# Performance work log

Hardware: AMD Instinct MI355X
Metric: run time of the kernel (lower is better)

The kernel has to match this reference:

```python
import jax, jax.numpy as jnp
import numpy as np

B, L, D = 16, 1024, 256  # batch, c_len == q_len (required by the expand/add in the source), 2*d_model


def mask_logits(x, m):
    # Faithful to the source's (unusual) masking: x*m + x*(1-m)*1e30
    return x * m + x * (1.0 - m) * 1e30


def setup_inputs() -> dict:
    key = jax.random.key(0)
    k = jax.random.split(key, 7)
    c = jax.random.normal(k[0], (B, L, D), dtype=jnp.float32)
    q = jax.random.normal(k[1], (B, L, D), dtype=jnp.float32)
    c_mask = jnp.ones((B, 1, L), dtype=jnp.float32)
    q_mask = jnp.ones((B, 1, L), dtype=jnp.float32)
    # Learned parameters (nn.Parameter zeros in the source; random here so the test is non-degenerate)
    c_weight = jax.random.normal(k[2], (D, 1), dtype=jnp.float32) * 0.05
    q_weight = jax.random.normal(k[3], (D, 1), dtype=jnp.float32) * 0.05
    cq_weight = jax.random.normal(k[4], (1, 1, D), dtype=jnp.float32) * 0.05
    bias = jnp.zeros((1,), dtype=jnp.float32)
    return {"c": c, "q": q, "c_mask": c_mask, "q_mask": q_mask,
            "c_weight": c_weight, "q_weight": q_weight,
            "cq_weight": cq_weight, "bias": bias}


def reference(c, q, c_mask, q_mask, c_weight, q_weight, cq_weight, bias):
    # Dropout treated as identity (inference) for a deterministic reference.
    s0 = jnp.matmul(c, c_weight)                      # [B, L, 1] -> broadcasts over q_len
    s1 = jnp.swapaxes(jnp.matmul(c, q_weight), 1, 2)  # [B, 1, L] (source uses c here, not q)
    s2 = jnp.einsum('bid,bjd->bij', c * cq_weight, q) # [B, L, L]
    S = s0 + s1 + s2 + bias                           # trilinear similarity
    S1 = jax.nn.softmax(mask_logits(S, q_mask), axis=-1)              # [B, Lc, Lq]
    C2Q = jnp.matmul(S1, q)                                           # [B, Lc, D]
    # torch F.softmax with no dim on a 3D tensor defaults to dim=0 (legacy behavior) -> axis=0
    S2 = jax.nn.softmax(mask_logits(jnp.swapaxes(S, 1, 2), c_mask), axis=0)  # [B, Lq, Lc]
    S2 = jnp.matmul(S1, S2)                                           # [B, Lc, Lc]
    Q2C = jnp.matmul(S2, c)                                           # [B, Lc, D]
    # torch.cat default dim=0 -> [4B, Lc, D]
    return jnp.concatenate((c, C2Q, c * C2Q, c * Q2C), axis=0)
```

## Files before the change

kernel.cpp:

```cpp
#include <hip/hip_runtime.h>

typedef __bf16 bf16;
typedef _Float16 f16;
typedef __attribute__((ext_vector_type(8))) __bf16 bf16x8;
typedef __attribute__((ext_vector_type(4))) __bf16 bf16x4;
typedef __attribute__((ext_vector_type(8))) _Float16 f16x8;
typedef __attribute__((ext_vector_type(4))) _Float16 f16x4;
typedef __attribute__((ext_vector_type(4))) float f32x4;

constexpr int Bn = 16, Ln = 1024, Dn = 256;

__device__ __forceinline__ float maskf(float m) { return m + (1.0f - m) * 1e30f; }

__device__ __forceinline__ void gload16(const void* g, void* l) {
  __builtin_amdgcn_global_load_lds((const __attribute__((address_space(1))) void*)g,
                                   (__attribute__((address_space(3))) void*)l, 16, 0, 0);
}

__device__ __forceinline__ void stageB128(const bf16* __restrict__ B, int ldb, int k0,
                                          bf16* lB, int tid, int wid) {
#pragma unroll
  for (int p = 0; p < 2; ++p) {
    int c0 = tid + (p << 8);
    int row = c0 >> 2, kk = (c0 & 3) << 3;
    gload16(B + (size_t)row * ldb + k0 + kk, lB + ((p << 8) + (wid << 6)) * 8);
  }
}

__device__ __forceinline__ void stageSwz64(const bf16* __restrict__ G, int ldg, int k0,
                                           bf16* L, int tid, int wid) {
#pragma unroll
  for (int p = 0; p < 2; ++p) {
    int u = tid + (p << 8);
    int row = u >> 3, s = u & 7;
    int kk = ((s ^ (row & 7)) << 3);
    gload16(G + (size_t)row * ldg + k0 + kk, L + ((p << 8) + (wid << 6)) * 8);
  }
}
__device__ __forceinline__ void stageSwz128(const bf16* __restrict__ G, int ldg, int k0,
                                            bf16* L, int tid, int wid) {
#pragma unroll
  for (int p = 0; p < 4; ++p) {
    int u = tid + (p << 8);
    int row = u >> 3, s = u & 7;
    int kk = ((s ^ (row & 7)) << 3);
    gload16(G + (size_t)row * ldg + k0 + kk, L + ((p << 8) + (wid << 6)) * 8);
  }
}

__device__ __forceinline__ const bf16* swzp(const bf16* L, int row, int slot) {
  return L + row * 64 + ((slot ^ (row & 7)) << 3);
}

__global__ __launch_bounds__(256) void k_prep2(
    const float* __restrict__ c, const float* __restrict__ q,
    const float* __restrict__ cw, const float* __restrict__ qw,
    const float* __restrict__ cqw, bf16* __restrict__ cm, bf16* __restrict__ qb,
    bf16* __restrict__ cT, bf16* __restrict__ qT,
    float* __restrict__ s0, float* __restrict__ s1, float* __restrict__ outc) {
  __shared__ __align__(16) bf16 tc[32][264];
  __shared__ __align__(16) bf16 tq[32][264];
  int blk = blockIdx.x;
  int b = blk >> 5;
  int l0 = (blk & 31) << 5;
  int t = threadIdx.x;
  int rl = t >> 3;
  int c0 = (t & 7) << 5;
  int grow = b * Ln + l0 + rl;
  size_t base = (size_t)grow * Dn + c0;
  float4 cv[8], qv[8];
#pragma unroll
  for (int k = 0; k < 8; ++k) {
    cv[k] = *(const float4*)&c[base + k * 4];
    qv[k] = *(const float4*)&q[base + k * 4];
  }
  float d0 = 0.f, d1 = 0.f;
#pragma unroll
  for (int k = 0; k < 8; ++k) {
    float4 w = *(const float4*)&cw[c0 + k * 4];
    float4 u = *(const float4*)&qw[c0 + k * 4];
    d0 += cv[k].x * w.x + cv[k].y * w.y + cv[k].z * w.z + cv[k].w * w.w;
    d1 += cv[k].x * u.x + cv[k].y * u.y + cv[k].z * u.z + cv[k].w * u.w;
  }
  d0 += __shfl_xor(d0, 1); d0 += __shfl_xor(d0, 2); d0 += __shfl_xor(d0, 4);
  d1 += __shfl_xor(d1, 1); d1 += __shfl_xor(d1, 2); d1 += __shfl_xor(d1, 4);
  if ((t & 7) == 0) { s0[grow] = d0; s1[grow] = d1; }
#pragma unroll
  for (int k = 0; k < 8; ++k) *(float4*)&outc[base + k * 4] = cv[k];
#pragma unroll
  for (int k2 = 0; k2 < 4; ++k2) {
    float4 m0 = *(const float4*)&cqw[c0 + k2 * 8];
    float4 m1 = *(const float4*)&cqw[c0 + k2 * 8 + 4];
    bf16x8 vm, vq, vc;
#pragma unroll
    for (int e = 0; e < 8; ++e) {
      float cvv = ((const float*)&cv[k2 * 2 + (e >> 2)])[e & 3];
      float qvv = ((const float*)&qv[k2 * 2 + (e >> 2)])[e & 3];
      float mw = (e < 4) ? ((const float*)&m0)[e] : ((const float*)&m1)[e - 4];
      vm[e] = (bf16)(cvv * mw);
      vq[e] = (bf16)qvv;
      vc[e] = (bf16)cvv;
    }
    *(bf16x8*)&cm[base + k2 * 8] = vm;
    *(bf16x8*)&qb[base + k2 * 8] = vq;
    *(bf16x8*)&tc[rl][c0 + k2 * 8] = vc;
    *(bf16x8*)&tq[rl][c0 + k2 * 8] = vq;
  }
  __syncthreads();
  int d = t;
  size_t tb = ((size_t)b * Dn + d) * Ln + l0;
  bf16x8 o[4];
#pragma unroll
  for (int j = 0; j < 4; ++j)
#pragma unroll
    for (int e = 0; e < 8; ++e) o[j][e] = tc[j * 8 + e][d];
#pragma unroll
  for (int j = 0; j < 4; ++j) *(bf16x8*)&cT[tb + j * 8] = o[j];
#pragma unroll
  for (int j = 0; j < 4; ++j)
#pragma unroll
    for (int e = 0; e < 8; ++e) o[j][e] = tq[j * 8 + e][d];
#pragma unroll
  for (int j = 0; j < 4; ++j) *(bf16x8*)&qT[tb + j * 8] = o[j];
}

__global__ __launch_bounds__(256) void g_s(const bf16* __restrict__ Am,
                                           const bf16* __restrict__ Bm,
                                           const float* __restrict__ s0,
                                           const float* __restrict__ s1,
                                           const float* __restrict__ bias,
                                           f16* __restrict__ S) {
  __shared__ __align__(16) bf16 lds[2][256 * 32];
  int f = blockIdx.x;
  int o = (f & 7) * 128 + (f >> 3);
  int bx = o & 7, by = (o >> 3) & 7, b = o >> 6;
  const bf16* Ab = Am + (size_t)b * Ln * Dn + (size_t)by * 128 * Dn;
  const bf16* Bb = Bm + (size_t)b * Ln * Dn + (size_t)bx * 128 * Dn;
  const int tid = threadIdx.x, wid = tid >> 6, lane = tid & 63;
  const int r = lane & 15, h = lane >> 4, wr = wid >> 1, wc = wid & 1;
  f32x4 acc[4][4];
  f32x4 zero = {0.f, 0.f, 0.f, 0.f};
#pragma unroll
  for (int i = 0; i < 4; ++i)
#pragma unroll
    for (int j = 0; j < 4; ++j) acc[i][j] = zero;

  stageB128(Ab, Dn, 0, &lds[0][0], tid, wid);
  stageB128(Bb, Dn, 0, &lds[0][128 * 32], tid, wid);
  __syncthreads();
  for (int t = 0; t < 8; ++t) {
    int cur = t & 1;
    if (t < 7) {
      stageB128(Ab, Dn, (t + 1) * 32, &lds[cur ^ 1][0], tid, wid);
      stageB128(Bb, Dn, (t + 1) * 32, &lds[cur ^ 1][128 * 32], tid, wid);
    }
    const bf16* lA = &lds[cur][0];
    const bf16* lB = &lds[cur][128 * 32];
    bf16x8 av[4], bv[4];
#pragma unroll
    for (int i = 0; i < 4; ++i) {
      av[i] = *(const bf16x8*)(lA + ((wr << 6) + (i << 4) + r) * 32 + (h << 3));
      bv[i] = *(const bf16x8*)(lB + ((wc << 6) + (i << 4) + r) * 32 + (h << 3));
    }
#pragma unroll
    for (int i = 0; i < 4; ++i)
#pragma unroll
      for (int j = 0; j < 4; ++j)
        acc[i][j] = __builtin_amdgcn_mfma_f32_16x16x32_bf16(av[i], bv[j], acc[i][j], 0, 0, 0);
    __syncthreads();
  }
  int grow = by * 128 + wr * 64, gcol = bx * 128 + wc * 64;
  float bvv = bias[0];
  size_t sb = (size_t)b * Ln * Ln;
#pragma unroll
  for (int j = 0; j < 4; ++j) {
    int n = gcol + j * 16 + r;
    float v1 = s1[b * Ln + n];
#pragma unroll
    for (int i = 0; i < 4; ++i) {
      int mb = grow + i * 16 + h * 4;
#pragma unroll
      for (int g = 0; g < 4; ++g) {
        float v0 = s0[b * Ln + mb + g];
        S[sb + (size_t)(mb + g) * Ln + n] = (f16)(acc[i][j][g] + v0 + v1 + bvv);
      }
    }
  }
}

__global__ __launch_bounds__(256) void k_rowsoftmax(const f16* __restrict__ S,
                                                    const float* __restrict__ qmask,
                                                    bf16* __restrict__ P1) {
  int t = threadIdx.x;
  int row = blockIdx.x * 4 + (t >> 6);
  int b = row >> 10;
  int lane = t & 63;
  const f16* Sr = S + (size_t)row * Ln;
  const float* qm = qmask + (size_t)b * Ln;
  float v[16];
  float mx = -3.4e38f;
#pragma unroll
  for (int p = 0; p < 2; ++p) {
    f16x8 x = ((const f16x8*)Sr)[lane + (p << 6)];
    float4 m0 = ((const float4*)qm)[(lane + (p << 6)) * 2];
    float4 m1 = ((const float4*)qm)[(lane + (p << 6)) * 2 + 1];
    float mm[8] = {m0.x, m0.y, m0.z, m0.w, m1.x, m1.y, m1.z, m1.w};
#pragma unroll
    for (int e = 0; e < 8; ++e) {
      float xv = (float)x[e] * maskf(mm[e]);
      v[8 * p + e] = xv;
      mx = fmaxf(mx, xv);
    }
  }
#pragma unroll
  for (int off = 32; off; off >>= 1) mx = fmaxf(mx, __shfl_xor(mx, off));
  float sum = 0.f;
#pragma unroll
  for (int k = 0; k < 16; ++k) {
    v[k] = __expf(v[k] - mx);
    sum += v[k];
  }
#pragma unroll
  for (int off = 32; off; off >>= 1) sum += __shfl_xor(sum, off);
  float inv = 1.0f / sum;
  bf16* Pr = P1 + (size_t)row * Ln;
#pragma unroll
  for (int p = 0; p < 2; ++p) {
    bf16x8 o;
#pragma unroll
    for (int e = 0; e < 8; ++e) o[e] = (bf16)(v[8 * p + e] * inv);
    ((bf16x8*)Pr)[lane + (p << 6)] = o;
  }
}

__global__ __launch_bounds__(256) void k_bp2(const f16* __restrict__ S,
                                             const float* __restrict__ cmask,
                                             bf16* __restrict__ P2) {
  __shared__ __align__(16) bf16 tile[16][32][36];
  int i0 = blockIdx.y * 32, j0 = blockIdx.x * 32;
  int t = threadIdx.x;
  int ti = t >> 3, tj4 = (t & 7) << 2;
  int i = i0 + ti;
  const f16* Sp = S + (size_t)i * Ln + j0 + tj4;
  float fm[16];
#pragma unroll
  for (int b = 0; b < 16; ++b) fm[b] = maskf(cmask[b * Ln + i]);
  float m[4] = {-3.4e38f, -3.4e38f, -3.4e38f, -3.4e38f};
#pragma unroll
  for (int b = 0; b < 16; ++b) {
    f16x4 u = *(const f16x4*)(Sp + (size_t)b * Ln * Ln);
#pragma unroll
    for (int g = 0; g < 4; ++g) m[g] = fmaxf(m[g], (float)u[g] * fm[b]);
  }
  float s[4] = {0.f, 0.f, 0.f, 0.f};
#pragma unroll
  for (int b = 0; b < 16; ++b) {
    f16x4 u = *(const f16x4*)(Sp + (size_t)b * Ln * Ln);
#pragma unroll
    for (int g = 0; g < 4; ++g) s[g] += __expf((float)u[g] * fm[b] - m[g]);
  }
#pragma unroll
  for (int g = 0; g < 4; ++g) s[g] = 1.0f / s[g];
#pragma unroll
  for (int b = 0; b < 16; ++b) {
    f16x4 u = *(const f16x4*)(Sp + (size_t)b * Ln * Ln);
#pragma unroll
    for (int g = 0; g < 4; ++g)
      tile[b][tj4 + g][ti] = (bf16)(__expf((float)u[g] * fm[b] - m[g]) * s[g]);
  }
  __syncthreads();
  int jl = t >> 3, i4 = (t & 7) << 2;
#pragma unroll
  for (int b = 0; b < 16; ++b) {
    *(bf16x4*)&P2[((size_t)b * Ln + j0 + jl) * Ln + i0 + i4] =
        *(const bf16x4*)&tile[b][jl][i4];
  }
}

__global__ __launch_bounds__(256) void g_t(const bf16* __restrict__ cT,
                                           const bf16* __restrict__ P2,
                                           bf16* __restrict__ TT) {
  __shared__ __align__(16) bf16 lds[2][192 * 64];
  int f = blockIdx.x;
  int o = (f & 7) * 64 + (f >> 3);
  int b = o >> 5, md = (o >> 3) & 3, nb = o & 7;
  const bf16* Ab = cT + (size_t)b * Dn * Ln + (size_t)md * 64 * Ln;
  const bf16* Bb = P2 + (size_t)b * Ln * Ln + (size_t)nb * 128 * Ln;
  const int tid = threadIdx.x, wid = tid >> 6, lane = tid & 63;
  const int r = lane & 15, h = lane >> 4, wr = wid >> 1, wc = wid & 1;
  f32x4 acc[2][4];
  f32x4 zero = {0.f, 0.f, 0.f, 0.f};
#pragma unroll
  for (int i = 0; i < 2; ++i)
#pragma unroll
    for (int j = 0; j < 4; ++j) acc[i][j] = zero;

  stageSwz64(Ab, Ln, 0, &lds[0][0], tid, wid);
  stageSwz128(Bb, Ln, 0, &lds[0][64 * 64], tid, wid);
  __syncthreads();
  for (int t = 0; t < 16; ++t) {
    int cur = t & 1;
    if (t < 15) {
      stageSwz64(Ab, Ln, (t + 1) * 64, &lds[cur ^ 1][0], tid, wid);
      stageSwz128(Bb, Ln, (t + 1) * 64, &lds[cur ^ 1][64 * 64], tid, wid);
    }
    const bf16* lA = &lds[cur][0];
    const bf16* lB = &lds[cur][64 * 64];
#pragma unroll
    for (int kk2 = 0; kk2 < 2; ++kk2) {
      int slot = (kk2 << 2) | h;
      bf16x8 av[2], bv[4];
#pragma unroll
      for (int i = 0; i < 2; ++i)
        av[i] = *(const bf16x8*)swzp(lA, (wr << 5) + (i << 4) + r, slot);
#pragma unroll
      for (int j = 0; j < 4; ++j)
        bv[j] = *(const bf16x8*)swzp(lB, (wc << 6) + (j << 4) + r, slot);
#pragma unroll
      for (int i = 0; i < 2; ++i)
#pragma unroll
        for (int j = 0; j < 4; ++j)
          acc[i][j] = __builtin_amdgcn_mfma_f32_16x16x32_bf16(av[i], bv[j], acc[i][j], 0, 0, 0);
    }
    __syncthreads();
  }
  size_t ob = (size_t)b * Dn * Ln;
  int dbase = md * 64 + wr * 32, cbase = nb * 128 + wc * 64;
#pragma unroll
  for (int i = 0; i < 2; ++i)
#pragma unroll
    for (int j = 0; j < 4; ++j) {
      int n = cbase + j * 16 + r;
#pragma unroll
      for (int g = 0; g < 4; ++g)
        TT[ob + (size_t)(dbase + i * 16 + h * 4 + g) * Ln + n] = (bf16)acc[i][j][g];
    }
}

__global__ __launch_bounds__(256) void g_cq(const bf16* __restrict__ P1,
                                            const bf16* __restrict__ qT,
                                            const bf16* __restrict__ TT,
                                            const float* __restrict__ c,
                                            float* __restrict__ out) {
  __shared__ __align__(16) bf16 lds[2][192 * 64];
  int f = blockIdx.x;
  int o = (f & 7) * 128 + (f >> 3);
  int b = o >> 6, by = (o >> 2) & 15, bx = o & 3;
  const bf16* Ab = P1 + (size_t)b * Ln * Ln + (size_t)by * 64 * Ln;
  const bf16* B1 = qT + (size_t)b * Dn * Ln + (size_t)bx * 64 * Ln;
  const bf16* B2 = TT + (size_t)b * Dn * Ln + (size_t)bx * 64 * Ln;
  const int tid = threadIdx.x, wid = tid >> 6, lane = tid & 63;
  const int r = lane & 15, h = lane >> 4, wr = wid >> 1, wc = wid & 1;
  f32x4 acc1[2][2], acc2[2][2];
  f32x4 zero = {0.f, 0.f, 0.f, 0.f};
#pragma unroll
  for (int i = 0; i < 2; ++i)
#pragma unroll
    for (int j = 0; j < 2; ++j) { acc1[i][j] = zero; acc2[i][j] = zero; }

  stageSwz64(Ab, Ln, 0, &lds[0][0], tid, wid);
  stageSwz64(B1, Ln, 0, &lds[0][4096], tid, wid);
  stageSwz64(B2, Ln, 0, &lds[0][8192], tid, wid);
  __syncthreads();
  for (int t = 0; t < 16; ++t) {
    int cur = t & 1;
    if (t < 15) {
      stageSwz64(Ab, Ln, (t + 1) * 64, &lds[cur ^ 1][0], tid, wid);
      stageSwz64(B1, Ln, (t + 1) * 64, &lds[cur ^ 1][4096], tid, wid);
      stageSwz64(B2, Ln, (t + 1) * 64, &lds[cur ^ 1][8192], tid, wid);
    }
    const bf16* lA = &lds[cur][0];
    const bf16* lB1 = &lds[cur][4096];
    const bf16* lB2 = &lds[cur][8192];
#pragma unroll
    for (int kk2 = 0; kk2 < 2; ++kk2) {
      int slot = (kk2 << 2) | h;
      bf16x8 av[2], bv[2];
#pragma unroll
      for (int i = 0; i < 2; ++i)
        av[i] = *(const bf16x8*)swzp(lA, (wr << 5) + (i << 4) + r, slot);
#pragma unroll
      for (int j = 0; j < 2; ++j)
        bv[j] = *(const bf16x8*)swzp(lB1, (wc << 5) + (j << 4) + r, slot);
#pragma unroll
      for (int i = 0; i < 2; ++i)
#pragma unroll
        for (int j = 0; j < 2; ++j)
          acc1[i][j] = __builtin_amdgcn_mfma_f32_16x16x32_bf16(av[i], bv[j], acc1[i][j], 0, 0, 0);
#pragma unroll
      for (int j = 0; j < 2; ++j)
        bv[j] = *(const bf16x8*)swzp(lB2, (wc << 5) + (j << 4) + r, slot);
#pragma unroll
      for (int i = 0; i < 2; ++i)
#pragma unroll
        for (int j = 0; j < 2; ++j)
          acc2[i][j] = __builtin_amdgcn_mfma_f32_16x16x32_bf16(av[i], bv[j], acc2[i][j], 0, 0, 0);
    }
    __syncthreads();
  }

  int grow = by * 64 + wr * 32, gcol = bx * 64 + wc * 32;
  const float* cb = c + (size_t)b * Ln * Dn;
  float* o1 = out + (size_t)(1 * Bn + b) * Ln * Dn;
  float* o2 = out + (size_t)(2 * Bn + b) * Ln * Dn;
  float* o3 = out + (size_t)(3 * Bn + b) * Ln * Dn;
#pragma unroll
  for (int j = 0; j < 2; ++j) {
    int n = gcol + j * 16 + r;
#pragma unroll
    for (int i = 0; i < 2; ++i) {
      int mb = grow + i * 16 + h * 4;
#pragma unroll
      for (int g = 0; g < 4; ++g) {
        float v1 = acc1[i][j][g];
        float v2 = acc2[i][j][g];
        size_t off = (size_t)(mb + g) * Dn + n;
        float cc = cb[off];
        o1[off] = v1;
        o2[off] = cc * v1;
        o3[off] = cc * v2;
      }
    }
  }
}

extern "C" void kernel_launch(void* const* d_in, const int* in_sizes, int n_in,
                              void* d_out, int out_size, void* d_ws, size_t ws_size,
                              hipStream_t stream) {
  const float* c = (const float*)d_in[0];
  const float* q = (const float*)d_in[1];
  const float* cmask = (const float*)d_in[2];
  const float* qmask = (const float*)d_in[3];
  const float* cw = (const float*)d_in[4];
  const float* qw = (const float*)d_in[5];
  const float* cqw = (const float*)d_in[6];
  const float* bias = (const float*)d_in[7];
  float* out = (float*)d_out;

  char* w = (char*)d_ws;
  f16* S = (f16*)w;       w += (size_t)Bn * Ln * Ln * 2;
  bf16* P1 = (bf16*)w;    w += (size_t)Bn * Ln * Ln * 2;
  bf16* P2 = (bf16*)w;    w += (size_t)Bn * Ln * Ln * 2;
  bf16* cm = (bf16*)w;    w += (size_t)Bn * Ln * Dn * 2;
  bf16* qb = (bf16*)w;    w += (size_t)Bn * Ln * Dn * 2;
  bf16* cT = (bf16*)w;    w += (size_t)Bn * Dn * Ln * 2;
  bf16* qT = (bf16*)w;    w += (size_t)Bn * Dn * Ln * 2;
  bf16* TT = (bf16*)w;    w += (size_t)Bn * Dn * Ln * 2;
  float* s0 = (float*)w;  w += (size_t)Bn * Ln * 4;
  float* s1 = (float*)w;  w += (size_t)Bn * Ln * 4;
  if ((size_t)(w - (char*)d_ws) > ws_size) return;

  k_prep2<<<dim3(Bn * Ln / 32), 256, 0, stream>>>(c, q, cw, qw, cqw, cm, qb, cT, qT, s0, s1, out);
  g_s<<<dim3(1024), 256, 0, stream>>>(cm, qb, s0, s1, bias, S);
  k_rowsoftmax<<<dim3(Bn * Ln / 4), 256, 0, stream>>>(S, qmask, P1);
  k_bp2<<<dim3(Ln / 32, Ln / 32), 256, 0, stream>>>(S, cmask, P2);
  g_t<<<dim3(512), 256, 0, stream>>>(cT, P2, TT);
  g_cq<<<dim3(1024), 256, 0, stream>>>(P1, qT, TT, c, out);
}
```

Before: 122.6 us.

## Use partial vmcnt waits so next-tile LDS loads overlap MFMA compute

The three GEMM kernels replace __syncthreads (which drains all outstanding global->LDS loads) with explicit s_waitcnt vmcnt(N) plus a raw barrier. Each iteration now waits only for the current buffer's loads while the prefetch of the next tile stays in flight during the MFMAs. Separately, the column-softmax kernel loads the 16 batch slices once into registers and reuses the exp values instead of reloading and recomputing them three times. The hand-counted vmcnt values must match the exact number of issued loads per stage, and the change raises register use in k_bp2.

```diff
diff --git a/kernel.cpp b/kernel.cpp
--- a/kernel.cpp
+++ b/kernel.cpp
@@ -16,6 +16,15 @@
   __builtin_amdgcn_global_load_lds((const __attribute__((address_space(1))) void*)g,
                                    (__attribute__((address_space(3))) void*)l, 16, 0, 0);
 }
+
+#define VMCNT(N) asm volatile("s_waitcnt vmcnt(" #N ")" ::: "memory")
+#define LGKM0 asm volatile("s_waitcnt lgkmcnt(0)" ::: "memory")
+#define BARR                                  \
+  do {                                        \
+    asm volatile("" ::: "memory");            \
+    __builtin_amdgcn_s_barrier();             \
+    asm volatile("" ::: "memory");            \
+  } while (0)
 
 __device__ __forceinline__ void stageB128(const bf16* __restrict__ B, int ldb, int k0,
                                           bf16* lB, int tid, int wid) {
@@ -147,13 +156,16 @@
 
   stageB128(Ab, Dn, 0, &lds[0][0], tid, wid);
   stageB128(Bb, Dn, 0, &lds[0][128 * 32], tid, wid);
-  __syncthreads();
   for (int t = 0; t < 8; ++t) {
     int cur = t & 1;
     if (t < 7) {
       stageB128(Ab, Dn, (t + 1) * 32, &lds[cur ^ 1][0], tid, wid);
       stageB128(Bb, Dn, (t + 1) * 32, &lds[cur ^ 1][128 * 32], tid, wid);
-    }
+      VMCNT(4);
+    } else {
+      VMCNT(0);
+    }
+    BARR;
     const bf16* lA = &lds[cur][0];
     const bf16* lB = &lds[cur][128 * 32];
     bf16x8 av[4], bv[4];
@@ -167,7 +179,7 @@
 #pragma unroll
       for (int j = 0; j < 4; ++j)
         acc[i][j] = __builtin_amdgcn_mfma_f32_16x16x32_bf16(av[i], bv[j], acc[i][j], 0, 0, 0);
-    __syncthreads();
+    LGKM0; BARR;
   }
   int grow = by * 128 + wr * 64, gcol = bx * 128 + wc * 64;
   float bvv = bias[0];
@@ -245,29 +257,29 @@
   float fm[16];
 #pragma unroll
   for (int b = 0; b < 16; ++b) fm[b] = maskf(cmask[b * Ln + i]);
+  f16x4 u[16];
+#pragma unroll
+  for (int b = 0; b < 16; ++b) u[b] = *(const f16x4*)(Sp + (size_t)b * Ln * Ln);
   float m[4] = {-3.4e38f, -3.4e38f, -3.4e38f, -3.4e38f};
 #pragma unroll
-  for (int b = 0; b < 16; ++b) {
-    f16x4 u = *(const f16x4*)(Sp + (size_t)b * Ln * Ln);
-#pragma unroll
-    for (int g = 0; g < 4; ++g) m[g] = fmaxf(m[g], (float)u[g] * fm[b]);
-  }
+  for (int b = 0; b < 16; ++b)
+#pragma unroll
+    for (int g = 0; g < 4; ++g) m[g] = fmaxf(m[g], (float)u[b][g] * fm[b]);
+  float e[16][4];
   float s[4] = {0.f, 0.f, 0.f, 0.f};
 #pragma unroll
-  for (int b = 0; b < 16; ++b) {
-    f16x4 u = *(const f16x4*)(Sp + (size_t)b * Ln * Ln);
-#pragma unroll
-    for (int g = 0; g < 4; ++g) s[g] += __expf((float)u[g] * fm[b] - m[g]);
-  }
+  for (int b = 0; b < 16; ++b)
+#pragma unroll
+    for (int g = 0; g < 4; ++g) {
+      e[b][g] = __expf((float)u[b][g] * fm[b] - m[g]);
+      s[g] += e[b][g];
+    }
 #pragma unroll
   for (int g = 0; g < 4; ++g) s[g] = 1.0f / s[g];
 #pragma unroll
-  for (int b = 0; b < 16; ++b) {
-    f16x4 u = *(const f16x4*)(Sp + (size_t)b * Ln * Ln);
-#pragma unroll
-    for (int g = 0; g < 4; ++g)
-      tile[b][tj4 + g][ti] = (bf16)(__expf((float)u[g] * fm[b] - m[g]) * s[g]);
-  }
+  for (int b = 0; b < 16; ++b)
+#pragma unroll
+    for (int g = 0; g < 4; ++g) tile[b][tj4 + g][ti] = (bf16)(e[b][g] * s[g]);
   __syncthreads();
   int jl = t >> 3, i4 = (t & 7) << 2;
 #pragma unroll
@@ -297,13 +309,16 @@
 
   stageSwz64(Ab, Ln, 0, &lds[0][0], tid, wid);
   stageSwz128(Bb, Ln, 0, &lds[0][64 * 64], tid, wid);
-  __syncthreads();
   for (int t = 0; t < 16; ++t) {
     int cur = t & 1;
     if (t < 15) {
       stageSwz64(Ab, Ln, (t + 1) * 64, &lds[cur ^ 1][0], tid, wid);
       stageSwz128(Bb, Ln, (t + 1) * 64, &lds[cur ^ 1][64 * 64], tid, wid);
-    }
+      VMCNT(6);
+    } else {
+      VMCNT(0);
+    }
+    BARR;
     const bf16* lA = &lds[cur][0];
     const bf16* lB = &lds[cur][64 * 64];
 #pragma unroll
@@ -322,7 +337,7 @@
         for (int j = 0; j < 4; ++j)
           acc[i][j] = __builtin_amdgcn_mfma_f32_16x16x32_bf16(av[i], bv[j], acc[i][j], 0, 0, 0);
     }
-    __syncthreads();
+    LGKM0; BARR;
   }
   size_t ob = (size_t)b * Dn * Ln;
   int dbase = md * 64 + wr * 32, cbase = nb * 128 + wc * 64;
@@ -361,14 +376,17 @@
   stageSwz64(Ab, Ln, 0, &lds[0][0], tid, wid);
   stageSwz64(B1, Ln, 0, &lds[0][4096], tid, wid);
   stageSwz64(B2, Ln, 0, &lds[0][8192], tid, wid);
-  __syncthreads();
   for (int t = 0; t < 16; ++t) {
     int cur = t & 1;
     if (t < 15) {
       stageSwz64(Ab, Ln, (t + 1) * 64, &lds[cur ^ 1][0], tid, wid);
       stageSwz64(B1, Ln, (t + 1) * 64, &lds[cur ^ 1][4096], tid, wid);
       stageSwz64(B2, Ln, (t + 1) * 64, &lds[cur ^ 1][8192], tid, wid);
-    }
+      VMCNT(6);
+    } else {
+      VMCNT(0);
+    }
+    BARR;
     const bf16* lA = &lds[cur][0];
     const bf16* lB1 = &lds[cur][4096];
     const bf16* lB2 = &lds[cur][8192];
@@ -396,7 +414,7 @@
         for (int j = 0; j < 2; ++j)
           acc2[i][j] = __builtin_amdgcn_mfma_f32_16x16x32_bf16(av[i], bv[j], acc2[i][j], 0, 0, 0);
     }
-    __syncthreads();
+    LGKM0; BARR;
   }
 
   int grow = by * 64 + wr * 32, gcol = bx * 64 + wc * 32;
```

Result: faster. 118.8 us (-3.1%).
